# Kernel optimization log

Measured on AMD Instinct MI355X. Metric: run time of the kernel, lower is better.

The kernel has to match this reference:

```python
import jax, jax.numpy as jnp
import numpy as np

SEQ_LEN, BSZ, EMBED_DIM, NDIM = 4096, 8, 1024, 16


def setup_inputs() -> dict:
    key = jax.random.key(0)
    k1, k2, k3, k4, k5, k6 = jax.random.split(key, 6)
    x = jax.random.normal(k1, (SEQ_LEN, BSZ, EMBED_DIM), dtype=jnp.float32)
    # delta pre-exp in (0.001, 0.1) as in reset_parameters
    delta = jax.random.uniform(k2, (EMBED_DIM, 1, 1), minval=0.001, maxval=0.1, dtype=jnp.float32)
    # alpha in (0.1, 1.5) guarantees q = 1 - p*alpha in (0, 1) -> stable log(q)
    alpha = jax.random.uniform(k3, (EMBED_DIM, NDIM, 1), minval=0.1, maxval=1.5, dtype=jnp.float32)
    beta = 1.0 + 0.02 * jax.random.normal(k4, (EMBED_DIM, NDIM, 1), dtype=jnp.float32)
    gamma = jax.random.normal(k5, (EMBED_DIM, NDIM), dtype=jnp.float32)
    omega = jax.random.normal(k6, (EMBED_DIM,), dtype=jnp.float32)
    return {"x": x, "delta": delta, "alpha": alpha, "beta": beta, "gamma": gamma, "omega": omega}


def reference(x, delta, alpha, beta, gamma, omega):
    # x: (L, B, D)
    L = x.shape[0]
    residual = x * omega  # broadcast over channel
    xt = jnp.transpose(x, (1, 2, 0))  # (B, D, L)

    # calc_params
    d = jnp.exp(delta)                      # (D, 1, 1)
    p = d / (1.0 + 0.5 * d * alpha)         # (D, N, 1)
    q = 1.0 - p * alpha                     # (D, N, 1), in (0,1)

    # compute_kernel: vander = arange(L) * log(q); k = einsum('dnl,dn->dl', p*beta*exp(vander), gamma)
    t = jnp.arange(L, dtype=x.dtype)[None, None, :]     # (1, 1, L)
    kernel = p * beta * jnp.exp(t * jnp.log(q))         # (D, N, L)
    k = jnp.einsum('dnl,dn->dl', kernel, gamma)         # (D, L)

    # causal FFT convolution with double-length padding
    n = 2 * L
    k_f = jnp.fft.rfft(k, n=n)              # (D, n//2+1)
    x_f = jnp.fft.rfft(xt, n=n)             # (B, D, n//2+1)
    out = jnp.fft.irfft(x_f * k_f, n=n)[..., :L]  # (B, D, L)

    return jnp.transpose(out, (2, 0, 1)) + residual  # (L, B, D)
```

## Files before the change

### kernel.cpp

```cpp
#include <hip/hip_runtime.h>


#define L_SEQ   4096
#define BSZ     8
#define EMBED   1024
#define NDIM    16
#define LC      256
#define WARM    64
#define NCHUNK  (L_SEQ / LC)
#define ROWSTR  (BSZ * EMBED)
#define T       16
#define NRING   4
#define DPB     256

__device__ __forceinline__ void gload_lds16(const float* src, float* dst_lds) {
    __builtin_amdgcn_global_load_lds(
        (const __attribute__((address_space(1))) void*)src,
        (__attribute__((address_space(3))) void*)dst_lds,
        16, 0, 0);
}

__global__ __launch_bounds__(256, 4) void ema_chunk_kernel(
    const float* __restrict__ x,
    const float* __restrict__ delta,
    const float* __restrict__ alpha,
    const float* __restrict__ beta,
    const float* __restrict__ gamma,
    const float* __restrict__ omega,
    float* __restrict__ out)
{
    __shared__ float lds[NRING][T][DPB];

    const int bid  = blockIdx.x;
    const int c    = bid % NCHUNK;
    const int tmp  = bid / NCHUNK;
    const int b    = tmp % BSZ;
    const int dg   = tmp / BSZ;
    const int tid  = threadIdx.x;
    const int wv   = tid >> 6;
    const int lane = tid & 63;
    const int d    = dg * DPB + tid;

    float q[NDIM], w[NDIM], s[NDIM];
    const float dd = expf(delta[d]);
    const float4* a4 = (const float4*)(alpha + (size_t)d * NDIM);
    const float4* b4 = (const float4*)(beta  + (size_t)d * NDIM);
    const float4* g4 = (const float4*)(gamma + (size_t)d * NDIM);
    #pragma unroll
    for (int v = 0; v < NDIM / 4; ++v) {
        const float4 av = a4[v], bv = b4[v], gv = g4[v];
        const float aa[4] = {av.x, av.y, av.z, av.w};
        const float bb[4] = {bv.x, bv.y, bv.z, bv.w};
        const float gg[4] = {gv.x, gv.y, gv.z, gv.w};
        #pragma unroll
        for (int j = 0; j < 4; ++j) {
            const int n = v * 4 + j;
            const float p = dd / (1.0f + 0.5f * dd * aa[j]);
            q[n] = 1.0f - p * aa[j];
            w[n] = p * bb[j] * gg[j];
            s[n] = 0.0f;
        }
    }

    const int l0    = c * LC;
    const int lw    = (l0 >= WARM) ? (l0 - WARM) : 0;
    const int woff  = l0 - lw;
    const int nbuf  = (woff + LC) / T;
    const int wB    = woff / T;

    const float om = omega[d];
    const float* xbase = x   + (size_t)lw * ROWSTR + (size_t)b * EMBED + (size_t)dg * DPB;
    float*       op    = out + (size_t)l0 * ROWSTR + (size_t)b * EMBED + d;
    const int lane4 = lane << 2;

    #define STAGE(kk)                                                        \
        if ((kk) < nbuf) {                                                   \
            const float* srow = xbase + (size_t)((kk) * T + wv * 4) * ROWSTR \
                                      + lane4;                               \
            float* drow = &lds[(kk) & (NRING - 1)][wv * 4][0];               \
            _Pragma("unroll")                                                \
            for (int r = 0; r < 4; ++r)                                      \
                gload_lds16(srow + (size_t)r * ROWSTR, drow + r * DPB);      \
        }

    STAGE(0)
    STAGE(1)
    STAGE(2)

    for (int k = 0; k < nbuf; ++k) {
        if (k <= wB) {
            asm volatile("s_waitcnt vmcnt(8)" ::: "memory");
        } else if (k == nbuf - 1) {
            asm volatile("s_waitcnt vmcnt(16)" ::: "memory");
        } else if (k == nbuf - 2) {
            asm volatile("s_waitcnt vmcnt(20)" ::: "memory");
        } else {
            asm volatile("s_waitcnt vmcnt(24)" ::: "memory");
        }
        __builtin_amdgcn_s_barrier();

        const int sl = k & (NRING - 1);
        if (k >= wB) {
            const int outbase = k * T - woff;
            #pragma unroll
            for (int r = 0; r < T; ++r) {
                const float xv = lds[sl][r][tid];
                float y0 = 0.0f, y1 = 0.0f;
                #pragma unroll
                for (int n = 0; n < NDIM; n += 2) {
                    s[n]     = fmaf(q[n],     s[n],     xv);
                    s[n + 1] = fmaf(q[n + 1], s[n + 1], xv);
                    y0 = fmaf(w[n],     s[n],     y0);
                    y1 = fmaf(w[n + 1], s[n + 1], y1);
                }
                __builtin_nontemporal_store(fmaf(om, xv, y0 + y1),
                                            &op[(size_t)(outbase + r) * ROWSTR]);
            }
        } else {
            #pragma unroll
            for (int r = 0; r < T; ++r) {
                const float xv = lds[sl][r][tid];
                #pragma unroll
                for (int n = 0; n < NDIM; ++n)
                    s[n] = fmaf(q[n], s[n], xv);
            }
        }

        __builtin_amdgcn_s_barrier();
        STAGE(k + 3)
    }
    #undef STAGE
}

extern "C" void kernel_launch(void* const* d_in, const int* in_sizes, int n_in,
                              void* d_out, int out_size, void* d_ws, size_t ws_size,
                              hipStream_t stream) {
    const float* x     = (const float*)d_in[0];
    const float* delta = (const float*)d_in[1];
    const float* alpha = (const float*)d_in[2];
    const float* beta  = (const float*)d_in[3];
    const float* gamma = (const float*)d_in[4];
    const float* omega = (const float*)d_in[5];
    float* out = (float*)d_out;

    const int blocks = NCHUNK * BSZ * (EMBED / DPB);
    ema_chunk_kernel<<<blocks, 256, 0, stream>>>(x, delta, alpha, beta, gamma, omega, out);
}
```

Measured before the change: 54.74 us.

## Split EMA state dimension across half-waves with shuffle reduction and longer chunks

Each channel's 16 EMA states are now split across two half-wavefronts of 8 states each. The partial outputs are combined with a cross-lane shuffle, and each half stores alternate time rows. Blocks now cover 128 channels and 512-step chunks, so the warmup recomputation is amortised over more steps. The LDS staging pattern and the vmcnt waits are rewritten to match. This halves registers per thread and shortens the serial dependency chain, at the cost of extra shuffles and duplicated x reads.

```diff
diff --git a/kernel.cpp b/kernel.cpp
--- a/kernel.cpp
+++ b/kernel.cpp
@@ -5,13 +5,14 @@
 #define BSZ     8
 #define EMBED   1024
 #define NDIM    16
-#define LC      256
+#define NH      8
+#define LC      512
 #define WARM    64
 #define NCHUNK  (L_SEQ / LC)
 #define ROWSTR  (BSZ * EMBED)
 #define T       16
 #define NRING   4
-#define DPB     256
+#define DPB     128
 
 __device__ __forceinline__ void gload_lds16(const float* src, float* dst_lds) {
     __builtin_amdgcn_global_load_lds(
@@ -39,15 +40,18 @@
     const int tid  = threadIdx.x;
     const int wv   = tid >> 6;
     const int lane = tid & 63;
-    const int d    = dg * DPB + tid;
+    const int half = lane >> 5;
+    const int dl   = wv * 32 + (lane & 31);
+    const int d    = dg * DPB + dl;
 
-    float q[NDIM], w[NDIM], s[NDIM];
+    float q[NH], w[NH], s[NH];
     const float dd = expf(delta[d]);
-    const float4* a4 = (const float4*)(alpha + (size_t)d * NDIM);
-    const float4* b4 = (const float4*)(beta  + (size_t)d * NDIM);
-    const float4* g4 = (const float4*)(gamma + (size_t)d * NDIM);
+    const size_t pb = (size_t)d * NDIM + (size_t)half * NH;
+    const float4* a4 = (const float4*)(alpha + pb);
+    const float4* b4 = (const float4*)(beta  + pb);
+    const float4* g4 = (const float4*)(gamma + pb);
     #pragma unroll
-    for (int v = 0; v < NDIM / 4; ++v) {
+    for (int v = 0; v < NH / 4; ++v) {
         const float4 av = a4[v], bv = b4[v], gv = g4[v];
         const float aa[4] = {av.x, av.y, av.z, av.w};
         const float bb[4] = {bv.x, bv.y, bv.z, bv.w};
@@ -71,16 +75,18 @@
     const float om = omega[d];
     const float* xbase = x   + (size_t)lw * ROWSTR + (size_t)b * EMBED + (size_t)dg * DPB;
     float*       op    = out + (size_t)l0 * ROWSTR + (size_t)b * EMBED + d;
-    const int lane4 = lane << 2;
 
     #define STAGE(kk)                                                        \
         if ((kk) < nbuf) {                                                   \
-            const float* srow = xbase + (size_t)((kk) * T + wv * 4) * ROWSTR \
-                                      + lane4;                               \
-            float* drow = &lds[(kk) & (NRING - 1)][wv * 4][0];               \
             _Pragma("unroll")                                                \
-            for (int r = 0; r < 4; ++r)                                      \
-                gload_lds16(srow + (size_t)r * ROWSTR, drow + r * DPB);      \
+            for (int j = 0; j < 2; ++j) {                                    \
+                const int row = wv * 4 + 2 * j;                              \
+                const float* src = xbase                                     \
+                    + (size_t)((kk) * T + row + half) * ROWSTR               \
+                    + ((lane & 31) << 2);                                    \
+                float* dstb = &lds[(kk) & (NRING - 1)][row][0];              \
+                gload_lds16(src, dstb);                                      \
+            }                                                                \
         }
 
     STAGE(0)
@@ -88,40 +94,45 @@
     STAGE(2)
 
     for (int k = 0; k < nbuf; ++k) {
-        if (k <= wB) {
-            asm volatile("s_waitcnt vmcnt(8)" ::: "memory");
-        } else if (k == nbuf - 1) {
-            asm volatile("s_waitcnt vmcnt(16)" ::: "memory");
-        } else if (k == nbuf - 2) {
-            asm volatile("s_waitcnt vmcnt(20)" ::: "memory");
-        } else {
-            asm volatile("s_waitcnt vmcnt(24)" ::: "memory");
-        }
+        if (k == nbuf - 1)      { asm volatile("s_waitcnt vmcnt(16)" ::: "memory"); }
+        else if (k == nbuf - 2) { asm volatile("s_waitcnt vmcnt(18)" ::: "memory"); }
+        else if (k <= wB)       { asm volatile("s_waitcnt vmcnt(4)"  ::: "memory"); }
+        else if (k == wB + 1)   { asm volatile("s_waitcnt vmcnt(12)" ::: "memory"); }
+        else                    { asm volatile("s_waitcnt vmcnt(20)" ::: "memory"); }
         __builtin_amdgcn_s_barrier();
 
         const int sl = k & (NRING - 1);
         if (k >= wB) {
             const int outbase = k * T - woff;
             #pragma unroll
-            for (int r = 0; r < T; ++r) {
-                const float xv = lds[sl][r][tid];
+            for (int r2 = 0; r2 < T; r2 += 2) {
+                const float xv0 = lds[sl][r2][dl];
+                const float xv1 = lds[sl][r2 + 1][dl];
                 float y0 = 0.0f, y1 = 0.0f;
                 #pragma unroll
-                for (int n = 0; n < NDIM; n += 2) {
-                    s[n]     = fmaf(q[n],     s[n],     xv);
-                    s[n + 1] = fmaf(q[n + 1], s[n + 1], xv);
-                    y0 = fmaf(w[n],     s[n],     y0);
-                    y1 = fmaf(w[n + 1], s[n + 1], y1);
+                for (int n = 0; n < NH; ++n) {
+                    s[n] = fmaf(q[n], s[n], xv0);
+                    y0   = fmaf(w[n], s[n], y0);
                 }
-                __builtin_nontemporal_store(fmaf(om, xv, y0 + y1),
-                                            &op[(size_t)(outbase + r) * ROWSTR]);
+                #pragma unroll
+                for (int n = 0; n < NH; ++n) {
+                    s[n] = fmaf(q[n], s[n], xv1);
+                    y1   = fmaf(w[n], s[n], y1);
+                }
+                y0 += __shfl_xor(y0, 32, 64);
+                y1 += __shfl_xor(y1, 32, 64);
+                y0 = fmaf(om, xv0, y0);
+                y1 = fmaf(om, xv1, y1);
+                const float yst = half ? y1 : y0;
+                __builtin_nontemporal_store(
+                    yst, &op[(size_t)(outbase + r2 + half) * ROWSTR]);
             }
         } else {
             #pragma unroll
             for (int r = 0; r < T; ++r) {
-                const float xv = lds[sl][r][tid];
+                const float xv = lds[sl][r][dl];
                 #pragma unroll
-                for (int n = 0; n < NDIM; ++n)
+                for (int n = 0; n < NH; ++n)
                     s[n] = fmaf(q[n], s[n], xv);
             }
         }
```

After: 58.03 us. 6.0% more time.

## Make LDS staging per-wave private and drop workgroup barriers

Applied to the files above, without the earlier changes.

Each wave now loads only the 64-channel slice of x it consumes into its own LDS region, so the ring buffer no longer needs block-wide s_barrier synchronization. The vmcnt wait thresholds are recomputed to account for the stores issued per step. This removes barrier stalls between waves, so each wave can run ahead independently. In exchange, correctness now rests on the hand-tuned vmcnt counts, since nothing else orders the async LDS loads against the reads.

```diff
diff --git a/kernel.cpp b/kernel.cpp
--- a/kernel.cpp
+++ b/kernel.cpp
@@ -12,6 +12,7 @@
 #define T       16
 #define NRING   4
 #define DPB     256
+#define DPW     64
 
 __device__ __forceinline__ void gload_lds16(const float* src, float* dst_lds) {
     __builtin_amdgcn_global_load_lds(
@@ -29,7 +30,7 @@
     const float* __restrict__ omega,
     float* __restrict__ out)
 {
-    __shared__ float lds[NRING][T][DPB];
+    __shared__ float lds[NRING][4][T][DPW];
 
     const int bid  = blockIdx.x;
     const int c    = bid % NCHUNK;
@@ -39,7 +40,7 @@
     const int tid  = threadIdx.x;
     const int wv   = tid >> 6;
     const int lane = tid & 63;
-    const int d    = dg * DPB + tid;
+    const int d    = dg * DPB + wv * DPW + lane;
 
     float q[NDIM], w[NDIM], s[NDIM];
     const float dd = expf(delta[d]);
@@ -69,18 +70,20 @@
     const int wB    = woff / T;
 
     const float om = omega[d];
-    const float* xbase = x   + (size_t)lw * ROWSTR + (size_t)b * EMBED + (size_t)dg * DPB;
+    const float* xbase = x + (size_t)lw * ROWSTR + (size_t)b * EMBED
+                           + (size_t)dg * DPB + (size_t)wv * DPW;
     float*       op    = out + (size_t)l0 * ROWSTR + (size_t)b * EMBED + d;
-    const int lane4 = lane << 2;
+    const int rsel = lane >> 4;
+    const int csel = (lane & 15) << 2;
 
     #define STAGE(kk)                                                        \
         if ((kk) < nbuf) {                                                   \
-            const float* srow = xbase + (size_t)((kk) * T + wv * 4) * ROWSTR \
-                                      + lane4;                               \
-            float* drow = &lds[(kk) & (NRING - 1)][wv * 4][0];               \
+            const float* sb = xbase + (size_t)((kk) * T) * ROWSTR;           \
+            float* db = &lds[(kk) & (NRING - 1)][wv][0][0];                  \
             _Pragma("unroll")                                                \
-            for (int r = 0; r < 4; ++r)                                      \
-                gload_lds16(srow + (size_t)r * ROWSTR, drow + r * DPB);      \
+            for (int i = 0; i < 4; ++i)                                      \
+                gload_lds16(sb + (size_t)(4 * i + rsel) * ROWSTR + csel,     \
+                            db + i * (4 * DPW));                             \
         }
 
     STAGE(0)
@@ -88,23 +91,18 @@
     STAGE(2)
 
     for (int k = 0; k < nbuf; ++k) {
-        if (k <= wB) {
-            asm volatile("s_waitcnt vmcnt(8)" ::: "memory");
-        } else if (k == nbuf - 1) {
-            asm volatile("s_waitcnt vmcnt(16)" ::: "memory");
-        } else if (k == nbuf - 2) {
-            asm volatile("s_waitcnt vmcnt(20)" ::: "memory");
-        } else {
-            asm volatile("s_waitcnt vmcnt(24)" ::: "memory");
-        }
-        __builtin_amdgcn_s_barrier();
+        if (k == nbuf - 1)      { asm volatile("s_waitcnt vmcnt(32)" ::: "memory"); }
+        else if (k == nbuf - 2) { asm volatile("s_waitcnt vmcnt(36)" ::: "memory"); }
+        else if (k <= wB)       { asm volatile("s_waitcnt vmcnt(8)"  ::: "memory"); }
+        else if (k == wB + 1)   { asm volatile("s_waitcnt vmcnt(24)" ::: "memory"); }
+        else                    { asm volatile("s_waitcnt vmcnt(40)" ::: "memory"); }
 
         const int sl = k & (NRING - 1);
         if (k >= wB) {
             const int outbase = k * T - woff;
             #pragma unroll
             for (int r = 0; r < T; ++r) {
-                const float xv = lds[sl][r][tid];
+                const float xv = lds[sl][wv][r][lane];
                 float y0 = 0.0f, y1 = 0.0f;
                 #pragma unroll
                 for (int n = 0; n < NDIM; n += 2) {
@@ -119,14 +117,13 @@
         } else {
             #pragma unroll
             for (int r = 0; r < T; ++r) {
-                const float xv = lds[sl][r][tid];
+                const float xv = lds[sl][wv][r][lane];
                 #pragma unroll
                 for (int n = 0; n < NDIM; ++n)
                     s[n] = fmaf(q[n], s[n], xv);
             }
         }
 
-        __builtin_amdgcn_s_barrier();
         STAGE(k + 3)
     }
     #undef STAGE
```

Measured after the change: 52.43 us. -4.2%, faster.
